# Kernel tuning notes

Hardware: AMD Instinct MI355X
Metric: run time of the kernel (lower is better)

The kernel has to match this reference:

```python
import jax, jax.numpy as jnp
import numpy as np

GAMMA = 0.01
INFER_STEP = 5


def softor(x, axis, gamma=GAMMA):
    # gamma * logsumexp(x / gamma) along `axis`, rescaled by global max if it exceeds 1
    y = gamma * jax.nn.logsumexp(x / gamma, axis=axis)
    mx = jnp.max(y)
    return jnp.where(mx > 1.0, y / mx, y)


def setup_inputs() -> dict:
    key = jax.random.key(0)
    k1, k2, k3 = jax.random.split(key, 3)
    B, G, C, S, L, m = 32, 2048, 16, 8, 3, 16
    x = jax.random.uniform(k1, (B, G), dtype=jnp.float32)          # valuation vector in [0,1]
    W = jax.random.normal(k2, (m, C), dtype=jnp.float32)           # clause-assignment weights
    I = jax.random.randint(k3, (C, G, S, L), 0, G)                 # index tensor into atom axis
    return {"x": x, "W": W, "I": I}


def reference(x, W, I):
    # x: [B,G] valuations; W: [m,C]; I: [C,G,S,L] int indices into G
    def r(V):
        # all C clause functions at once: gather V along atom axis using I
        gathered = V[:, I]                      # [B,C,G,S,L]
        body = jnp.prod(gathered, axis=-1)      # conjunction over body literals -> [B,C,G,S]
        Cv = softor(body, axis=-1)              # softor over substitutions -> [B,C,G]
        Ws = jax.nn.softmax(W, axis=1)          # [m,C]
        H = jnp.einsum('mc,bcg->mbg', Ws, Cv)   # weighted clause mix -> [m,B,G]
        return softor(H, axis=0)                # softor over m heads -> [B,G]

    R = x
    for _ in range(INFER_STEP):
        R = softor(jnp.stack([R, r(R)], axis=1), axis=1)  # amalgamate old and new facts
    return R
```

## Files before the change

### kernel.cpp

```cpp
#include <hip/hip_runtime.h>

#define GAMMA 0.01f
#define B 32
#define G 2048
#define C 16
#define S 8
#define L 3
#define M 16
#define NBLK 256
#define NTHR 512
#define GSTR 16

#define K_EXP 144.26950408889634f
#define K_LOG 0.006931471805599453f

#define SCOPE __HIP_MEMORY_SCOPE_AGENT

__device__ __forceinline__ void ast(unsigned* p, unsigned v) {
    __hip_atomic_store(p, v, __ATOMIC_RELAXED, SCOPE);
}
__device__ __forceinline__ float aldf(const float* p) {
    return __hip_atomic_load(p, __ATOMIC_RELAXED, SCOPE);
}
__device__ __forceinline__ void astf(float* p, float v) {
    __hip_atomic_store(p, v, __ATOMIC_RELAXED, SCOPE);
}
__device__ __forceinline__ unsigned long long ald64(const unsigned long long* p) {
    return __hip_atomic_load(p, __ATOMIC_RELAXED, SCOPE);
}
__device__ __forceinline__ void ast64(unsigned long long* p, unsigned long long v) {
    __hip_atomic_store(p, v, __ATOMIC_RELAXED, SCOPE);
}

__device__ __forceinline__ float waveMax(float v) {
#pragma unroll
    for (int off = 32; off > 0; off >>= 1)
        v = fmaxf(v, __shfl_xor(v, off, 64));
    return v;
}

__device__ __forceinline__ float red8(const float* s) {
    return fmaxf(fmaxf(fmaxf(s[0], s[1]), fmaxf(s[2], s[3])),
                 fmaxf(fmaxf(s[4], s[5]), fmaxf(s[6], s[7])));
}

__device__ __forceinline__ void barArrive(unsigned long long* slot, unsigned ep,
                                          float v, float* scratch) {
    asm volatile("s_waitcnt vmcnt(0) lgkmcnt(0)" ::: "memory");
    float wm = waveMax(v);
    __syncthreads();
    if ((threadIdx.x & 63) == 0) scratch[threadIdx.x >> 6] = wm;
    __syncthreads();
    if (threadIdx.x == 0) {
        float bm = red8(scratch);
        ast64(&slot[blockIdx.x], ((unsigned long long)ep << 32) |
                                 (unsigned long long)__float_as_uint(bm));
    }
}

__device__ __forceinline__ float barWait(const unsigned long long* slot,
                                         unsigned long long* gslot,
                                         unsigned ep, float* scratch) {
    const int t = threadIdx.x;
    if (t < 64) {
        if ((blockIdx.x & 15) == 0) {
            float pv = -INFINITY;
            if (t < 16) {
                unsigned long long got;
                int guard = 0;
                do { got = ald64(&slot[blockIdx.x + t]); }
                while ((unsigned)(got >> 32) < ep && ++guard < (1 << 17));
                pv = __uint_as_float((unsigned)got);
            }
            float gm = waveMax(pv);
            if (t == 0)
                ast64(&gslot[(size_t)(blockIdx.x >> 4) * GSTR],
                      ((unsigned long long)ep << 32) |
                      (unsigned long long)__float_as_uint(gm));
        }
        float qv = -INFINITY;
        if (t < 16) {
            unsigned long long got;
            int guard = 0;
            do { got = ald64(&gslot[(size_t)t * GSTR]); }
            while ((unsigned)(got >> 32) < ep && ++guard < (1 << 17));
            qv = __uint_as_float((unsigned)got);
        }
        float fm = waveMax(qv);
        if (t == 0) scratch[0] = fm;
    }
    __syncthreads();
    return scratch[0];
}

extern "C" __global__ __launch_bounds__(512, 2) void kmain(
    const float* __restrict__ x, const float* __restrict__ W,
    const int* __restrict__ I,
    unsigned long long* __restrict__ slotA, unsigned long long* __restrict__ slotB,
    unsigned long long* __restrict__ slotC, unsigned long long* __restrict__ gslotA,
    unsigned long long* __restrict__ gslotB, unsigned long long* __restrict__ gslotC,
    unsigned* __restrict__ Ipk, float* __restrict__ Ry, float* __restrict__ out)
{
    __shared__ __align__(16) float Vrow[G];
    __shared__ __align__(16) float WsL[C * M];
    __shared__ float ph[256 * 33];
    __shared__ float scratch[8];

    const int t = threadIdx.x;
    const int bid = blockIdx.x;
    const int b = bid & 31;
    const int gt = bid >> 5;
    const int ch = t >> 8;
    const int gl = t & 255;
    const int g = (gt << 8) + gl;

    if (t < 256) {
        const int m = t >> 4, c = t & 15;
        float rmax = -INFINITY;
#pragma unroll
        for (int j = 0; j < C; j++) rmax = fmaxf(rmax, W[m * C + j]);
        float rsum = 0.f;
#pragma unroll
        for (int j = 0; j < C; j++) rsum += __expf(W[m * C + j] - rmax);
        WsL[c * M + m] = __expf(W[m * C + c] - rmax) / rsum;
    }
    {
        const int tid = bid * NTHR + t;
        if (tid < C * G) {
            const int4* ip4 = (const int4*)(I + (size_t)tid * 24);
            int idx[24];
#pragma unroll
            for (int j = 0; j < 6; j++) {
                int4 v = ip4[j];
                idx[4 * j + 0] = v.x; idx[4 * j + 1] = v.y;
                idx[4 * j + 2] = v.z; idx[4 * j + 3] = v.w;
            }
            unsigned* dst = Ipk + (size_t)tid * 12;
#pragma unroll
            for (int j = 0; j < 12; j++)
                ast(&dst[j],
                    ((unsigned)idx[2 * j] << 2) | ((unsigned)idx[2 * j + 1] << 18));
        }
    }
    barArrive(slotC, 1, -INFINITY, scratch);
    float m3 = barWait(slotC, gslotC, 1, scratch);

    float ry = 0.f;
    for (int it = 0; it < 5; it++) {
        float s = 1.0f;
        if (it > 0)
            s = (m3 > 1.0f) ? 1.0f / m3 : 1.0f;
        if (it == 0) {
            const float4* V4 = (const float4*)(x + (size_t)b * G);
            ((float4*)Vrow)[t] = V4[t];
        } else {
            const float* src = Ry + (size_t)b * G;
#pragma unroll
            for (int j = 0; j < 4; j++) {
                const int gg = t + j * 512;
                Vrow[gg] = s * aldf(&src[gg]);
            }
        }
        __syncthreads();

        float h[M];
#pragma unroll
        for (int m = 0; m < M; m++) h[m] = 0.f;
        float ymax = -INFINITY;
        const char* vb = (const char*)Vrow;

#pragma unroll 2
        for (int cc = 0; cc < 8; cc++) {
            const int c = ch * 8 + cc;
            const uint4* ip = (const uint4*)(Ipk + ((size_t)c * G + g) * 12);
            uint4 u0 = ip[0], u1 = ip[1], u2 = ip[2];
            unsigned w[12] = {u0.x, u0.y, u0.z, u0.w, u1.x, u1.y,
                              u1.z, u1.w, u2.x, u2.y, u2.z, u2.w};
            float vv[24];
#pragma unroll
            for (int q = 0; q < 12; q++) {
                vv[2 * q]     = *(const float*)(vb + (w[q] & 0xffffu));
                vv[2 * q + 1] = *(const float*)(vb + (w[q] >> 16));
            }
            float body[S];
#pragma unroll
            for (int ss = 0; ss < S; ss++)
                body[ss] = vv[ss * 3] * vv[ss * 3 + 1] * vv[ss * 3 + 2];
            float bm = body[0];
#pragma unroll
            for (int ss = 1; ss < S; ss++) bm = fmaxf(bm, body[ss]);
            float sum = 0.f;
#pragma unroll
            for (int ss = 0; ss < S; ss++)
                sum += exp2f((body[ss] - bm) * K_EXP);
            float y = fmaf(K_LOG, log2f(sum), bm);
            ymax = fmaxf(ymax, y);
            const float4* Wc = (const float4*)&WsL[c * M];
            float4 w0 = Wc[0], w1 = Wc[1], w2 = Wc[2], w3 = Wc[3];
            const float wv[16] = {w0.x, w0.y, w0.z, w0.w, w1.x, w1.y, w1.z, w1.w,
                                  w2.x, w2.y, w2.z, w2.w, w3.x, w3.y, w3.z, w3.w};
#pragma unroll
            for (int m = 0; m < M; m++)
                h[m] = fmaf(wv[m], y, h[m]);
        }
#pragma unroll
        for (int m = 0; m < M; m++)
            ph[gl * 33 + ch * 16 + m] = h[m];
        barArrive(slotA, it + 1, ymax, scratch);
        float hraw[M];
        if (t < 256) {
#pragma unroll
            for (int m = 0; m < M; m++)
                hraw[m] = ph[t * 33 + m] + ph[t * 33 + 16 + m];
        }
        float m1 = barWait(slotA, gslotA, it + 1, scratch);

        float hy = -INFINITY;
        if (t < 256) {
            float s1 = (m1 > 1.0f) ? 1.0f / m1 : 1.0f;
            float hv[M];
            float hm = -INFINITY;
#pragma unroll
            for (int m = 0; m < M; m++) {
                hv[m] = s1 * hraw[m];
                hm = fmaxf(hm, hv[m]);
            }
            float sum = 0.f;
#pragma unroll
            for (int m = 0; m < M; m++) sum += exp2f((hv[m] - hm) * K_EXP);
            hy = fmaf(K_LOG, log2f(sum), hm);
        }
        barArrive(slotB, it + 1, hy, scratch);
        float Rv = (t < 256) ? Vrow[(gt << 8) + t] : 0.f;
        float m2 = barWait(slotB, gslotB, it + 1, scratch);

        float rt = -INFINITY;
        if (t < 256) {
            float s2 = (m2 > 1.0f) ? 1.0f / m2 : 1.0f;
            float rv = s2 * hy;
            float a = fmaxf(Rv, rv), d = fminf(Rv, rv);
            ry = fmaf(K_LOG, log2f(1.0f + exp2f((d - a) * K_EXP)), a);
            astf(&Ry[(size_t)b * G + (gt << 8) + t], ry);
            rt = ry;
        }
        barArrive(slotC, it + 2, rt, scratch);
        m3 = barWait(slotC, gslotC, it + 2, scratch);
    }

    if (t < 256) {
        float sf = (m3 > 1.0f) ? 1.0f / m3 : 1.0f;
        out[(size_t)b * G + (gt << 8) + t] = sf * ry;
    }
}

extern "C" void kernel_launch(void* const* d_in, const int* in_sizes, int n_in,
                              void* d_out, int out_size, void* d_ws, size_t ws_size,
                              hipStream_t stream) {
    const float* x = (const float*)d_in[0];
    const float* W = (const float*)d_in[1];
    const int*   I = (const int*)d_in[2];
    float* out = (float*)d_out;

    unsigned long long* slotA  = (unsigned long long*)d_ws;
    unsigned long long* slotB  = slotA + NBLK;
    unsigned long long* slotC  = slotB + NBLK;
    unsigned long long* gslotA = slotC + NBLK;
    unsigned long long* gslotB = gslotA + 16 * GSTR;
    unsigned long long* gslotC = gslotB + 16 * GSTR;
    float* Ry = (float*)(gslotC + 16 * GSTR);
    unsigned* Ipk = (unsigned*)(Ry + (size_t)B * G);

    hipMemsetAsync(slotA, 0, (3 * NBLK + 3 * 16 * GSTR) * sizeof(unsigned long long),
                   stream);

    kmain<<<dim3(NBLK), dim3(NTHR), 0, stream>>>(
        x, W, I, slotA, slotB, slotC, gslotA, gslotB, gslotC, Ipk, Ry, out);
}
```

Baseline: 146.0 us.

## Replace grid barrier with sibling waits and defer global-max rescale

The full grid barrier at the end of each iteration is replaced by a wait on only the 8 sibling blocks that produce the same batch row. The global-max rescale factor is applied algebraically after the gather: the body product scales by s^3, so the softor uses scaled exponents, and the global max is read later with a flat poll over all slots. This lets the gather and product work overlap with the global reduction. The cost is a fully unrolled 8x8 body buffer that raises register pressure, plus a second polling pass.

After: 164.6 us. 1.13x slower.

```diff
diff --git a/kernel.cpp b/kernel.cpp
--- a/kernel.cpp
+++ b/kernel.cpp
@@ -93,6 +93,42 @@
     return scratch[0];
 }
 
+__device__ __forceinline__ float flatWaitMax(const unsigned long long* slot,
+                                             unsigned ep, float* scratch) {
+    const int t = threadIdx.x;
+    if (t < 64) {
+        unsigned long long g0, g1, g2, g3;
+        int guard = 0;
+        for (;;) {
+            g0 = ald64(&slot[t * 4 + 0]); g1 = ald64(&slot[t * 4 + 1]);
+            g2 = ald64(&slot[t * 4 + 2]); g3 = ald64(&slot[t * 4 + 3]);
+            bool ready =
+                ((unsigned)(g0 >> 32) >= ep) && ((unsigned)(g1 >> 32) >= ep) &&
+                ((unsigned)(g2 >> 32) >= ep) && ((unsigned)(g3 >> 32) >= ep);
+            if (ready || ++guard >= (1 << 17)) break;
+            __builtin_amdgcn_s_sleep(1);
+        }
+        float pm = fmaxf(
+            fmaxf(__uint_as_float((unsigned)g0), __uint_as_float((unsigned)g1)),
+            fmaxf(__uint_as_float((unsigned)g2), __uint_as_float((unsigned)g3)));
+        pm = waveMax(pm);
+        if (t == 0) scratch[0] = pm;
+    }
+    __syncthreads();
+    return scratch[0];
+}
+
+__device__ __forceinline__ void siblingWait(const unsigned long long* slot,
+                                            unsigned ep, int b) {
+    if (threadIdx.x < 8) {
+        unsigned long long got;
+        int guard = 0;
+        do { got = ald64(&slot[b + 32 * (int)threadIdx.x]); }
+        while ((unsigned)(got >> 32) < ep && ++guard < (1 << 17));
+    }
+    __syncthreads();
+}
+
 extern "C" __global__ __launch_bounds__(512, 2) void kmain(
     const float* __restrict__ x, const float* __restrict__ W,
     const int* __restrict__ I,
@@ -143,33 +179,29 @@
         }
     }
     barArrive(slotC, 1, -INFINITY, scratch);
-    float m3 = barWait(slotC, gslotC, 1, scratch);
+    (void)barWait(slotC, gslotC, 1, scratch);
 
     float ry = 0.f;
+    float s = 1.0f;
     for (int it = 0; it < 5; it++) {
-        float s = 1.0f;
-        if (it > 0)
-            s = (m3 > 1.0f) ? 1.0f / m3 : 1.0f;
         if (it == 0) {
             const float4* V4 = (const float4*)(x + (size_t)b * G);
             ((float4*)Vrow)[t] = V4[t];
         } else {
+            siblingWait(slotC, it + 1, b);
             const float* src = Ry + (size_t)b * G;
 #pragma unroll
             for (int j = 0; j < 4; j++) {
                 const int gg = t + j * 512;
-                Vrow[gg] = s * aldf(&src[gg]);
+                Vrow[gg] = aldf(&src[gg]);
             }
         }
         __syncthreads();
 
-        float h[M];
-#pragma unroll
-        for (int m = 0; m < M; m++) h[m] = 0.f;
-        float ymax = -INFINITY;
+        float bodyv[8][8];
+        float bmv[8];
         const char* vb = (const char*)Vrow;
-
-#pragma unroll 2
+#pragma unroll
         for (int cc = 0; cc < 8; cc++) {
             const int c = ch * 8 + cc;
             const uint4* ip = (const uint4*)(Ipk + ((size_t)c * G + g) * 12);
@@ -182,18 +214,38 @@
                 vv[2 * q]     = *(const float*)(vb + (w[q] & 0xffffu));
                 vv[2 * q + 1] = *(const float*)(vb + (w[q] >> 16));
             }
-            float body[S];
 #pragma unroll
             for (int ss = 0; ss < S; ss++)
-                body[ss] = vv[ss * 3] * vv[ss * 3 + 1] * vv[ss * 3 + 2];
-            float bm = body[0];
-#pragma unroll
-            for (int ss = 1; ss < S; ss++) bm = fmaxf(bm, body[ss]);
+                bodyv[cc][ss] = vv[ss * 3] * vv[ss * 3 + 1] * vv[ss * 3 + 2];
+            float bm = bodyv[cc][0];
+#pragma unroll
+            for (int ss = 1; ss < S; ss++) bm = fmaxf(bm, bodyv[cc][ss]);
+            bmv[cc] = bm;
+        }
+        __builtin_amdgcn_sched_barrier(0);
+
+        if (it > 0) {
+            float m3v = flatWaitMax(slotC, it + 1, scratch);
+            s = (m3v > 1.0f) ? 1.0f / m3v : 1.0f;
+        } else {
+            s = 1.0f;
+        }
+        const float s3 = s * s * s;
+        const float ke = s3 * K_EXP;
+
+        float h[M];
+#pragma unroll
+        for (int m = 0; m < M; m++) h[m] = 0.f;
+        float ymax = -INFINITY;
+#pragma unroll
+        for (int cc = 0; cc < 8; cc++) {
+            const int c = ch * 8 + cc;
+            const float bm = bmv[cc];
             float sum = 0.f;
 #pragma unroll
             for (int ss = 0; ss < S; ss++)
-                sum += exp2f((body[ss] - bm) * K_EXP);
-            float y = fmaf(K_LOG, log2f(sum), bm);
+                sum += exp2f((bodyv[cc][ss] - bm) * ke);
+            float y = fmaf(K_LOG, log2f(sum), s3 * bm);
             ymax = fmaxf(ymax, y);
             const float4* Wc = (const float4*)&WsL[c * M];
             float4 w0 = Wc[0], w1 = Wc[1], w2 = Wc[2], w3 = Wc[3];
@@ -231,7 +283,7 @@
             hy = fmaf(K_LOG, log2f(sum), hm);
         }
         barArrive(slotB, it + 1, hy, scratch);
-        float Rv = (t < 256) ? Vrow[(gt << 8) + t] : 0.f;
+        float Rv = (t < 256) ? s * Vrow[(gt << 8) + t] : 0.f;
         float m2 = barWait(slotB, gslotB, it + 1, scratch);
 
         float rt = -INFINITY;
@@ -244,9 +296,9 @@
             rt = ry;
         }
         barArrive(slotC, it + 2, rt, scratch);
-        m3 = barWait(slotC, gslotC, it + 2, scratch);
-    }
-
+    }
+
+    float m3 = barWait(slotC, gslotC, 6, scratch);
     if (t < 256) {
         float sf = (m3 > 1.0f) ? 1.0f / m3 : 1.0f;
         out[(size_t)b * G + (gt << 8) + t] = sf * ry;
```
